# Optimization experiments

Measured on AMD Instinct MI355X. Metric: run time of the kernel, lower is better.

## Reference

```python
import jax, jax.numpy as jnp
import numpy as np
from jax import lax

# --- configuration matching init_kwargs ---
N = 512          # head_size: square cost matrices, marginals a=b=ones(N)
REG = 0.05       # entropy_reg
TAU = 1000.0     # absorption threshold on scaling vectors
N_ITER = 50      # max_iter (fixed iteration count; tol early-exit omitted)
BATCH = 128


def setup_inputs() -> dict:
    key = jax.random.key(0)
    # nonnegative cost matrices, uniform [0,1)
    X = jax.random.uniform(key, (BATCH, N, N), dtype=jnp.float32)
    return {"X": X}


def _sinkhorn_stabilized(M):
    """Log-stabilized Sinkhorn (POT sinkhorn_stabilized) for one cost matrix M [N,N].

    Marginals a = b = ones(N). Returns transport plan Gamma [N,N].
    """
    a = jnp.ones((N,), M.dtype)
    b = jnp.ones((N,), M.dtype)

    def step(carry, _):
        alpha, beta, u, v = carry
        # K = exp(-(M - alpha_i - beta_j)/reg)
        K = jnp.exp((alpha[:, None] + beta[None, :] - M) / REG)
        v = b / (K.T @ u)
        u = a / (K @ v)
        # tau-based absorption of large scalings into the log-domain potentials
        absorb = (jnp.max(jnp.abs(u)) > TAU) | (jnp.max(jnp.abs(v)) > TAU)
        alpha = jnp.where(absorb, alpha + REG * jnp.log(u), alpha)
        beta = jnp.where(absorb, beta + REG * jnp.log(v), beta)
        u = jnp.where(absorb, jnp.full_like(u, 1.0 / N), u)
        v = jnp.where(absorb, jnp.full_like(v, 1.0 / N), v)
        return (alpha, beta, u, v), None

    init = (
        jnp.zeros((N,), M.dtype),          # alpha
        jnp.zeros((N,), M.dtype),          # beta
        jnp.full((N,), 1.0 / N, M.dtype),  # u
        jnp.full((N,), 1.0 / N, M.dtype),  # v
    )
    (alpha, beta, u, v), _ = lax.scan(step, init, None, length=N_ITER)
    # Gamma = exp(-(M - alpha_i - beta_j)/reg + log u_i + log v_j)
    Gamma = jnp.exp(
        (alpha[:, None] + beta[None, :] - M) / REG
        + jnp.log(u)[:, None]
        + jnp.log(v)[None, :]
    )
    return Gamma


def reference(X):
    # original mutates X[i] in place per batch element; we return the batched result
    return jax.vmap(_sinkhorn_stabilized)(X)
```

## Files before the change

kernel.cpp:

```cpp
#include <hip/hip_runtime.h>

constexpr int BN = 512;
constexpr int NITER = 50;

#define CEXP  (-28.853900817779268f)
#define ESH   (14.0f)
#define L2TAU (9.965784284662087f)

typedef unsigned int u32;

__device__ __forceinline__ float fexp2(float x) { return __builtin_amdgcn_exp2f(x); }
__device__ __forceinline__ float flog2(float x) { return __builtin_amdgcn_logf(x); }

__device__ __forceinline__ float nr_rcp(float x) {
    float r = __builtin_amdgcn_rcpf(x);
    return fmaf(r, fmaf(-x, r, 1.0f), r);
}

template <int CTRL>
__device__ __forceinline__ float dppx(float x) {
    return __int_as_float(__builtin_amdgcn_update_dpp(
        0, __float_as_int(x), CTRL, 0xF, 0xF, true));
}

__device__ __forceinline__ float bfly_sum(float x) {
    x += dppx<0xB1>(x);
    x += dppx<0x4E>(x);
    x += dppx<0x141>(x);
    x += dppx<0x140>(x);
    x += __shfl_xor(x, 16, 64);
    x += __shfl_xor(x, 32, 64);
    return x;
}
__device__ __forceinline__ float bfly_max(float x) {
    x = fmaxf(x, dppx<0xB1>(x));
    x = fmaxf(x, dppx<0x4E>(x));
    x = fmaxf(x, dppx<0x141>(x));
    x = fmaxf(x, dppx<0x140>(x));
    x = fmaxf(x, __shfl_xor(x, 16, 64));
    x = fmaxf(x, __shfl_xor(x, 32, 64));
    return x;
}

__device__ __forceinline__ void fma_mix2(float& accLo, float& accHi, u32 e2,
                                         float pLo, float pHi) {
    asm("v_fma_mix_f32 %0, %2, %3, %0 op_sel_hi:[1,0,0]\n\t"
        "v_fma_mix_f32 %1, %2, %4, %1 op_sel:[1,0,0] op_sel_hi:[1,0,0]"
        : "+v"(accLo), "+v"(accHi)
        : "v"(e2), "v"(pLo), "v"(pHi));
}

__global__ __launch_bounds__(256)
void prep_exp_t(const float* __restrict__ X, float* __restrict__ out)
{
    const int blk  = blockIdx.x;
    const int b    = blk >> 4;
    const int tile = blk & 15;
    const int i0   = (tile >> 2) << 7;
    const int j0   = (tile & 3) << 7;
    const int tid  = threadIdx.x;

    const float* __restrict__ Mb = X + (size_t)b * (BN * BN);
    _Float16* __restrict__ Et = reinterpret_cast<_Float16*>(out + (size_t)b * (BN * BN));

    __shared__ _Float16 T[128][130];

    #pragma unroll
    for (int k = 0; k < 16; ++k) {
        int idx = tid + (k << 8);
        int fi  = idx >> 5;
        int fj  = idx & 31;
        float4 m = *reinterpret_cast<const float4*>(Mb + (size_t)(i0 + fi) * BN + j0 + (fj << 2));
        T[(fj << 2) + 0][fi] = (_Float16)fexp2(fmaf(m.x, CEXP, ESH));
        T[(fj << 2) + 1][fi] = (_Float16)fexp2(fmaf(m.y, CEXP, ESH));
        T[(fj << 2) + 2][fi] = (_Float16)fexp2(fmaf(m.z, CEXP, ESH));
        T[(fj << 2) + 3][fi] = (_Float16)fexp2(fmaf(m.w, CEXP, ESH));
    }
    __syncthreads();
    #pragma unroll
    for (int k = 0; k < 32; ++k) {
        int o  = tid + (k << 8);
        int j  = o >> 6;
        int c2 = o & 63;
        u32 val = *reinterpret_cast<const u32*>(&T[j][c2 << 1]);
        *reinterpret_cast<u32*>(Et + (size_t)(j0 + j) * BN + i0 + (c2 << 1)) = val;
    }
}

__global__ __launch_bounds__(1024, 4)
void sinkhorn_iter3(const float* __restrict__ X, float* __restrict__ out,
                    float* __restrict__ cucv)
{
    const int b    = blockIdx.x;
    const int t    = threadIdx.x;
    const int lane = t & 63;
    const int w    = t >> 6;

    const u32* __restrict__ Et4 =
        reinterpret_cast<const u32*>(out + (size_t)b * (BN * BN));

    __shared__ float ah[BN], bh[BN], lu[BN], lv[BN], pv[BN];
    __shared__ float tpart[8][BN];
    __shared__ float wmaxlu[8], wmaxlv[16];
    __shared__ uint4 stage[16][8][64];

    if (t < BN) {
        ah[t] = 0.f; bh[t] = 0.f;
        lu[t] = -9.f; lv[t] = -9.f;
        pv[t] = 0x1p-9f;
    }

    const int jb0 = w << 5;

    #pragma unroll
    for (int c = 0; c < 8; ++c)
        stage[w][c][lane] =
            *reinterpret_cast<const uint4*>(Et4 + (size_t)(jb0 + 24 + c) * 256 + (lane << 2));

    uint4 e[4], f[4];
    #pragma unroll
    for (int c = 0; c < 4; ++c)
        e[c] = *reinterpret_cast<const uint4*>(Et4 + (size_t)(jb0 + c) * 256 + (lane << 2));

    __syncthreads();

    for (int it = 0; it < NITER; ++it) {
        float pr[8];
        *reinterpret_cast<float4*>(&pr[0]) = *reinterpret_cast<const float4*>(&pv[lane * 8]);
        *reinterpret_cast<float4*>(&pr[4]) = *reinterpret_cast<const float4*>(&pv[lane * 8 + 4]);

        float acc[8] = {0, 0, 0, 0, 0, 0, 0, 0};
        float vml = -1e30f;

        auto dogroup = [&](const uint4* eg, int jb) {
            const float4 bh4 = *reinterpret_cast<const float4*>(&bh[jb]);
            float q[4], lvv[4];
            #pragma unroll
            for (int c = 0; c < 4; ++c) {
                float s0 = 0.f, s1 = 0.f;
                fma_mix2(s0, s1, eg[c].x, pr[0], pr[1]);
                fma_mix2(s0, s1, eg[c].y, pr[2], pr[3]);
                fma_mix2(s0, s1, eg[c].z, pr[4], pr[5]);
                fma_mix2(s0, s1, eg[c].w, pr[6], pr[7]);
                float s = bfly_sum(s0 + s1) * 0x1p-14f;
                q[c] = nr_rcp(s);
                const float bj = (c == 0) ? bh4.x : (c == 1) ? bh4.y : (c == 2) ? bh4.z : bh4.w;
                lvv[c] = -bj - flog2(s);
                vml = fmaxf(vml, lvv[c]);
            }
            if (lane == 0)
                *reinterpret_cast<float4*>(&lv[jb]) = make_float4(lvv[0], lvv[1], lvv[2], lvv[3]);
            #pragma unroll
            for (int c = 0; c < 4; ++c) {
                fma_mix2(acc[0], acc[1], eg[c].x, q[c], q[c]);
                fma_mix2(acc[2], acc[3], eg[c].y, q[c], q[c]);
                fma_mix2(acc[4], acc[5], eg[c].z, q[c], q[c]);
                fma_mix2(acc[6], acc[7], eg[c].w, q[c], q[c]);
            }
        };

        #pragma unroll
        for (int g = 0; g < 6; ++g) {
            const int jb = jb0 + (g << 2);
            const int jn = (g < 5) ? (jb + 4) : jb0;
            #pragma unroll
            for (int c = 0; c < 4; ++c)
                f[c] = *reinterpret_cast<const uint4*>(Et4 + (size_t)(jn + c) * 256 + (lane << 2));
            dogroup(e, jb);
            #pragma unroll
            for (int c = 0; c < 4; ++c) e[c] = f[c];
        }
        #pragma unroll
        for (int g = 0; g < 2; ++g) {
            uint4 el[4];
            #pragma unroll
            for (int c = 0; c < 4; ++c) el[c] = stage[w][(g << 2) + c][lane];
            dogroup(el, jb0 + 24 + (g << 2));
        }

        if (w < 8) {
            *reinterpret_cast<float4*>(&tpart[w][lane * 8]) =
                make_float4(acc[0], acc[1], acc[2], acc[3]);
            *reinterpret_cast<float4*>(&tpart[w][lane * 8 + 4]) =
                make_float4(acc[4], acc[5], acc[6], acc[7]);
        }
        if (lane == 0) wmaxlv[w] = vml;
        __syncthreads();
        if (w >= 8) {
            float4* p0 = reinterpret_cast<float4*>(&tpart[w - 8][lane * 8]);
            float4* p1 = reinterpret_cast<float4*>(&tpart[w - 8][lane * 8 + 4]);
            float4 o0 = *p0, o1 = *p1;
            o0.x += acc[0]; o0.y += acc[1]; o0.z += acc[2]; o0.w += acc[3];
            o1.x += acc[4]; o1.y += acc[5]; o1.z += acc[6]; o1.w += acc[7];
            *p0 = o0; *p1 = o1;
        }
        __syncthreads();

        float lun = 0.f, tt = 0.f;
        if (t < BN) {
            float p0 = 0, p1 = 0, p2 = 0, p3 = 0;
            #pragma unroll
            for (int w2 = 0; w2 < 8; w2 += 4) {
                p0 += tpart[w2 + 0][t];
                p1 += tpart[w2 + 1][t];
                p2 += tpart[w2 + 2][t];
                p3 += tpart[w2 + 3][t];
            }
            tt  = ((p0 + p1) + (p2 + p3)) * 0x1p-14f;
            lun = -ah[t] - flog2(tt);
            float m = bfly_max(lun);
            if (lane == 0) wmaxlu[w] = m;
        }
        __syncthreads();

        if (t < BN) {
            float mlu = wmaxlu[0], mlv = wmaxlv[0];
            #pragma unroll
            for (int i2 = 1; i2 < 8; ++i2)  mlu = fmaxf(mlu, wmaxlu[i2]);
            #pragma unroll
            for (int i2 = 1; i2 < 16; ++i2) mlv = fmaxf(mlv, wmaxlv[i2]);
            if (mlu > L2TAU || mlv > L2TAU) {
                float an = ah[t] + lun;
                ah[t] = an;
                lu[t] = -9.f;
                pv[t] = fexp2(an - 9.0f);
                bh[t] += lv[t];
                lv[t] = -9.f;
            } else {
                lu[t] = lun;
                pv[t] = nr_rcp(tt);
            }
        }
        __syncthreads();
    }

    if (cucv != nullptr) {
        if (t < BN) {
            cucv[(size_t)b * 1024 + t]       = ah[t] + lu[t];
            cucv[(size_t)b * 1024 + 512 + t] = bh[t] + lv[t];
        }
    } else {
        if (t < BN) {
            pv[t] = ah[t] + lu[t];
            lv[t] = bh[t] + lv[t];
        }
        __syncthreads();
        const int j  = t & 511;
        const int i0 = (t >> 9) * 256;
        const float cvj = lv[j];
        const float* __restrict__ Mb = X + (size_t)b * (BN * BN);
        float* __restrict__ Gb = out + (size_t)b * (BN * BN);
        #pragma unroll 4
        for (int i = i0; i < i0 + 256; ++i)
            Gb[(size_t)i * BN + j] = fexp2(fmaf(Mb[(size_t)i * BN + j], CEXP, pv[i] + cvj));
    }
}

__global__ __launch_bounds__(256)
void gamma_out(const float* __restrict__ X, float* __restrict__ out,
               const float* __restrict__ cucv)
{
    const int blk  = blockIdx.x;
    const int b    = blk >> 4;
    const int tile = blk & 15;
    const int tid  = threadIdx.x;
    const int i0   = tile << 5;

    __shared__ float cu[32];
    __shared__ float cv[BN];

    if (tid < 32) cu[tid] = cucv[(size_t)b * 1024 + i0 + tid];
    cv[tid]        = cucv[(size_t)b * 1024 + 512 + tid];
    cv[tid + 256]  = cucv[(size_t)b * 1024 + 768 + tid];
    __syncthreads();

    const float* __restrict__ Mb = X + (size_t)b * (BN * BN);
    float* __restrict__ Gb = out + (size_t)b * (BN * BN);
    const float4* __restrict__ cv4 = reinterpret_cast<const float4*>(cv);

    #pragma unroll
    for (int k = 0; k < 16; ++k) {
        int idx = tid + (k << 8);
        int r   = idx >> 7;
        int c4  = idx & 127;
        int i   = i0 + r;
        float4 m = *reinterpret_cast<const float4*>(Mb + (size_t)i * BN + (c4 << 2));
        float4 c = cv4[c4];
        float cui = cu[r];
        float4 g;
        g.x = fexp2(fmaf(m.x, CEXP, cui + c.x));
        g.y = fexp2(fmaf(m.y, CEXP, cui + c.y));
        g.z = fexp2(fmaf(m.z, CEXP, cui + c.z));
        g.w = fexp2(fmaf(m.w, CEXP, cui + c.w));
        *reinterpret_cast<float4*>(Gb + (size_t)i * BN + (c4 << 2)) = g;
    }
}

extern "C" void kernel_launch(void* const* d_in, const int* in_sizes, int n_in,
                              void* d_out, int out_size, void* d_ws, size_t ws_size,
                              hipStream_t stream)
{
    const float* X = (const float*)d_in[0];
    float* out = (float*)d_out;
    const int batch = in_sizes[0] / (BN * BN);

    prep_exp_t<<<batch * 16, 256, 0, stream>>>(X, out);

    const size_t cucv_bytes = (size_t)batch * 1024 * sizeof(float);
    if (ws_size >= cucv_bytes) {
        float* cucv = (float*)d_ws;
        sinkhorn_iter3<<<batch, 1024, 0, stream>>>(X, out, cucv);
        gamma_out<<<batch * 16, 256, 0, stream>>>(X, out, cucv);
    } else {
        sinkhorn_iter3<<<batch, 1024, 0, stream>>>(X, out, nullptr);
    }
}
```

Baseline: 709.2 us.

## Stream E tiles via async global-to-LDS double-buffered loads each iteration

Replaces the register-prefetch-plus-static-LDS-stage scheme with direct global_load_lds double buffering. Every iteration now streams all 8 groups of 4 rows per wave from global or L2 into LDS, instead of keeping a quarter of them resident in LDS. Plain barriers become an explicit lgkmcnt wait plus s_barrier. The aim is to cut VGPR pressure and overlap memory with compute. In exchange it adds more global traffic per iteration, and the vmcnt(4) wait is hand-tuned and could break if the compiler emits other vector-memory ops.

```diff
diff --git a/kernel.cpp b/kernel.cpp
--- a/kernel.cpp
+++ b/kernel.cpp
@@ -48,6 +48,16 @@
         "v_fma_mix_f32 %1, %2, %4, %1 op_sel:[1,0,0] op_sel_hi:[1,0,0]"
         : "+v"(accLo), "+v"(accHi)
         : "v"(e2), "v"(pLo), "v"(pHi));
+}
+
+__device__ __forceinline__ void gload16(const u32* g, void* l) {
+    __builtin_amdgcn_global_load_lds(
+        (const __attribute__((address_space(1))) u32*)g,
+        (__attribute__((address_space(3))) u32*)l, 16, 0, 0);
+}
+
+__device__ __forceinline__ void barrier_lgkm() {
+    asm volatile("s_waitcnt lgkmcnt(0)\n\ts_barrier" ::: "memory");
 }
 
 __global__ __launch_bounds__(256)
@@ -88,7 +98,7 @@
 }
 
 __global__ __launch_bounds__(1024, 4)
-void sinkhorn_iter3(const float* __restrict__ X, float* __restrict__ out,
+void sinkhorn_iter4(const float* __restrict__ X, float* __restrict__ out,
                     float* __restrict__ cucv)
 {
     const int b    = blockIdx.x;
@@ -102,27 +112,21 @@
     __shared__ float ah[BN], bh[BN], lu[BN], lv[BN], pv[BN];
     __shared__ float tpart[8][BN];
     __shared__ float wmaxlu[8], wmaxlv[16];
-    __shared__ uint4 stage[16][8][64];
+    __shared__ uint4 sbuf[16][2][4][64];
 
     if (t < BN) {
         ah[t] = 0.f; bh[t] = 0.f;
         lu[t] = -9.f; lv[t] = -9.f;
         pv[t] = 0x1p-9f;
     }
+    __syncthreads();
 
     const int jb0 = w << 5;
-
-    #pragma unroll
-    for (int c = 0; c < 8; ++c)
-        stage[w][c][lane] =
-            *reinterpret_cast<const uint4*>(Et4 + (size_t)(jb0 + 24 + c) * 256 + (lane << 2));
-
-    uint4 e[4], f[4];
+    const u32* gb = Et4 + (size_t)jb0 * 256 + (lane << 2);
+
     #pragma unroll
     for (int c = 0; c < 4; ++c)
-        e[c] = *reinterpret_cast<const uint4*>(Et4 + (size_t)(jb0 + c) * 256 + (lane << 2));
-
-    __syncthreads();
+        gload16(gb + c * 256, &sbuf[w][0][c][0]);
 
     for (int it = 0; it < NITER; ++it) {
         float pr[8];
@@ -132,50 +136,44 @@
         float acc[8] = {0, 0, 0, 0, 0, 0, 0, 0};
         float vml = -1e30f;
 
-        auto dogroup = [&](const uint4* eg, int jb) {
+        #pragma unroll
+        for (int g = 0; g < 8; ++g) {
+            const int nb   = (g + 1) & 7;
+            const int nbuf = (g + 1) & 1;
+            #pragma unroll
+            for (int c = 0; c < 4; ++c)
+                gload16(gb + (size_t)(nb * 4 + c) * 256, &sbuf[w][nbuf][c][0]);
+
+            asm volatile("s_waitcnt vmcnt(4)" ::: "memory");
+
+            const int jb = jb0 + (g << 2);
+            uint4 e[4];
+            #pragma unroll
+            for (int c = 0; c < 4; ++c) e[c] = sbuf[w][g & 1][c][lane];
+
             const float4 bh4 = *reinterpret_cast<const float4*>(&bh[jb]);
-            float q[4], lvv[4];
+            float q[4];
             #pragma unroll
             for (int c = 0; c < 4; ++c) {
                 float s0 = 0.f, s1 = 0.f;
-                fma_mix2(s0, s1, eg[c].x, pr[0], pr[1]);
-                fma_mix2(s0, s1, eg[c].y, pr[2], pr[3]);
-                fma_mix2(s0, s1, eg[c].z, pr[4], pr[5]);
-                fma_mix2(s0, s1, eg[c].w, pr[6], pr[7]);
+                fma_mix2(s0, s1, e[c].x, pr[0], pr[1]);
+                fma_mix2(s0, s1, e[c].y, pr[2], pr[3]);
+                fma_mix2(s0, s1, e[c].z, pr[4], pr[5]);
+                fma_mix2(s0, s1, e[c].w, pr[6], pr[7]);
                 float s = bfly_sum(s0 + s1) * 0x1p-14f;
                 q[c] = nr_rcp(s);
                 const float bj = (c == 0) ? bh4.x : (c == 1) ? bh4.y : (c == 2) ? bh4.z : bh4.w;
-                lvv[c] = -bj - flog2(s);
-                vml = fmaxf(vml, lvv[c]);
+                float lvj = -bj - flog2(s);
+                vml = fmaxf(vml, lvj);
+                if (lane == 0) lv[jb + c] = lvj;
             }
-            if (lane == 0)
-                *reinterpret_cast<float4*>(&lv[jb]) = make_float4(lvv[0], lvv[1], lvv[2], lvv[3]);
             #pragma unroll
             for (int c = 0; c < 4; ++c) {
-                fma_mix2(acc[0], acc[1], eg[c].x, q[c], q[c]);
-                fma_mix2(acc[2], acc[3], eg[c].y, q[c], q[c]);
-                fma_mix2(acc[4], acc[5], eg[c].z, q[c], q[c]);
-                fma_mix2(acc[6], acc[7], eg[c].w, q[c], q[c]);
+                fma_mix2(acc[0], acc[1], e[c].x, q[c], q[c]);
+                fma_mix2(acc[2], acc[3], e[c].y, q[c], q[c]);
+                fma_mix2(acc[4], acc[5], e[c].z, q[c], q[c]);
+                fma_mix2(acc[6], acc[7], e[c].w, q[c], q[c]);
             }
-        };
-
-        #pragma unroll
-        for (int g = 0; g < 6; ++g) {
-            const int jb = jb0 + (g << 2);
-            const int jn = (g < 5) ? (jb + 4) : jb0;
-            #pragma unroll
-            for (int c = 0; c < 4; ++c)
-                f[c] = *reinterpret_cast<const uint4*>(Et4 + (size_t)(jn + c) * 256 + (lane << 2));
-            dogroup(e, jb);
-            #pragma unroll
-            for (int c = 0; c < 4; ++c) e[c] = f[c];
-        }
-        #pragma unroll
-        for (int g = 0; g < 2; ++g) {
-            uint4 el[4];
-            #pragma unroll
-            for (int c = 0; c < 4; ++c) el[c] = stage[w][(g << 2) + c][lane];
-            dogroup(el, jb0 + 24 + (g << 2));
         }
 
         if (w < 8) {
@@ -185,7 +183,7 @@
                 make_float4(acc[4], acc[5], acc[6], acc[7]);
         }
         if (lane == 0) wmaxlv[w] = vml;
-        __syncthreads();
+        barrier_lgkm();
         if (w >= 8) {
             float4* p0 = reinterpret_cast<float4*>(&tpart[w - 8][lane * 8]);
             float4* p1 = reinterpret_cast<float4*>(&tpart[w - 8][lane * 8 + 4]);
@@ -194,7 +192,7 @@
             o1.x += acc[4]; o1.y += acc[5]; o1.z += acc[6]; o1.w += acc[7];
             *p0 = o0; *p1 = o1;
         }
-        __syncthreads();
+        barrier_lgkm();
 
         float lun = 0.f, tt = 0.f;
         if (t < BN) {
@@ -211,7 +209,7 @@
             float m = bfly_max(lun);
             if (lane == 0) wmaxlu[w] = m;
         }
-        __syncthreads();
+        barrier_lgkm();
 
         if (t < BN) {
             float mlu = wmaxlu[0], mlv = wmaxlv[0];
@@ -231,8 +229,10 @@
                 pv[t] = nr_rcp(tt);
             }
         }
-        __syncthreads();
-    }
+        barrier_lgkm();
+    }
+
+    asm volatile("s_waitcnt vmcnt(0)" ::: "memory");
 
     if (cucv != nullptr) {
         if (t < BN) {
@@ -309,9 +309,9 @@
     const size_t cucv_bytes = (size_t)batch * 1024 * sizeof(float);
     if (ws_size >= cucv_bytes) {
         float* cucv = (float*)d_ws;
-        sinkhorn_iter3<<<batch, 1024, 0, stream>>>(X, out, cucv);
+        sinkhorn_iter4<<<batch, 1024, 0, stream>>>(X, out, cucv);
         gamma_out<<<batch * 16, 256, 0, stream>>>(X, out, cucv);
     } else {
-        sinkhorn_iter3<<<batch, 1024, 0, stream>>>(X, out, nullptr);
-    }
-}
+        sinkhorn_iter4<<<batch, 1024, 0, stream>>>(X, out, nullptr);
+    }
+}
```

Result: slower. 900.9 us (+27.0%).

## Deepen global prefetch ring, shrink LDS staging, drop a barrier per iteration

Applied to the files above, without the earlier changes.

The per-wave matrix loop now keeps a three-group-deep register ring of prefetched global loads instead of a single double buffer. Fewer rows are staged in LDS (4 instead of 8), so more are streamed from global or L2 each iteration. All 16 waves write their partial column sums into a larger LDS buffer, which removes one barrier and the read-add-write reduction step. Barriers become a raw lgkmcnt wait plus s_barrier, and occupancy is pinned with waves_per_eu(4,4). The trade-off is higher register pressure from the ring and more global traffic per iteration, in exchange for more latency hiding and less synchronization.

```diff
diff --git a/kernel.cpp b/kernel.cpp
--- a/kernel.cpp
+++ b/kernel.cpp
@@ -48,6 +48,10 @@
         "v_fma_mix_f32 %1, %2, %4, %1 op_sel:[1,0,0] op_sel_hi:[1,0,0]"
         : "+v"(accLo), "+v"(accHi)
         : "v"(e2), "v"(pLo), "v"(pHi));
+}
+
+__device__ __forceinline__ void barrier_lgkm() {
+    asm volatile("s_waitcnt lgkmcnt(0)\n\ts_barrier" ::: "memory");
 }
 
 __global__ __launch_bounds__(256)
@@ -87,8 +91,9 @@
     }
 }
 
-__global__ __launch_bounds__(1024, 4)
-void sinkhorn_iter3(const float* __restrict__ X, float* __restrict__ out,
+__global__ __launch_bounds__(1024)
+__attribute__((amdgpu_waves_per_eu(4, 4)))
+void sinkhorn_iter5(const float* __restrict__ X, float* __restrict__ out,
                     float* __restrict__ cucv)
 {
     const int b    = blockIdx.x;
@@ -100,9 +105,9 @@
         reinterpret_cast<const u32*>(out + (size_t)b * (BN * BN));
 
     __shared__ float ah[BN], bh[BN], lu[BN], lv[BN], pv[BN];
-    __shared__ float tpart[8][BN];
+    __shared__ float tpart[16][BN];
     __shared__ float wmaxlu[8], wmaxlv[16];
-    __shared__ uint4 stage[16][8][64];
+    __shared__ uint4 stage[16][4][64];
 
     if (t < BN) {
         ah[t] = 0.f; bh[t] = 0.f;
@@ -113,14 +118,17 @@
     const int jb0 = w << 5;
 
     #pragma unroll
-    for (int c = 0; c < 8; ++c)
+    for (int c = 0; c < 4; ++c)
         stage[w][c][lane] =
-            *reinterpret_cast<const uint4*>(Et4 + (size_t)(jb0 + 24 + c) * 256 + (lane << 2));
-
-    uint4 e[4], f[4];
-    #pragma unroll
-    for (int c = 0; c < 4; ++c)
-        e[c] = *reinterpret_cast<const uint4*>(Et4 + (size_t)(jb0 + c) * 256 + (lane << 2));
+            *reinterpret_cast<const uint4*>(Et4 + (size_t)(jb0 + 28 + c) * 256 + (lane << 2));
+
+    uint4 ring[4][4];
+    #pragma unroll
+    for (int g = 0; g < 3; ++g)
+        #pragma unroll
+        for (int c = 0; c < 4; ++c)
+            ring[g][c] = *reinterpret_cast<const uint4*>(
+                Et4 + (size_t)(jb0 + (g << 2) + c) * 256 + (lane << 2));
 
     __syncthreads();
 
@@ -134,7 +142,7 @@
 
         auto dogroup = [&](const uint4* eg, int jb) {
             const float4 bh4 = *reinterpret_cast<const float4*>(&bh[jb]);
-            float q[4], lvv[4];
+            float q[4];
             #pragma unroll
             for (int c = 0; c < 4; ++c) {
                 float s0 = 0.f, s1 = 0.f;
@@ -145,11 +153,10 @@
                 float s = bfly_sum(s0 + s1) * 0x1p-14f;
                 q[c] = nr_rcp(s);
                 const float bj = (c == 0) ? bh4.x : (c == 1) ? bh4.y : (c == 2) ? bh4.z : bh4.w;
-                lvv[c] = -bj - flog2(s);
-                vml = fmaxf(vml, lvv[c]);
+                float lvj = -bj - flog2(s);
+                vml = fmaxf(vml, lvj);
+                if (lane == 0) lv[jb + c] = lvj;
             }
-            if (lane == 0)
-                *reinterpret_cast<float4*>(&lv[jb]) = make_float4(lvv[0], lvv[1], lvv[2], lvv[3]);
             #pragma unroll
             for (int c = 0; c < 4; ++c) {
                 fma_mix2(acc[0], acc[1], eg[c].x, q[c], q[c]);
@@ -160,47 +167,33 @@
         };
 
         #pragma unroll
-        for (int g = 0; g < 6; ++g) {
-            const int jb = jb0 + (g << 2);
-            const int jn = (g < 5) ? (jb + 4) : jb0;
+        for (int g = 0; g < 7; ++g) {
+            dogroup(ring[g & 3], jb0 + (g << 2));
+            const int gp = (g + 3) % 7;
             #pragma unroll
             for (int c = 0; c < 4; ++c)
-                f[c] = *reinterpret_cast<const uint4*>(Et4 + (size_t)(jn + c) * 256 + (lane << 2));
-            dogroup(e, jb);
-            #pragma unroll
-            for (int c = 0; c < 4; ++c) e[c] = f[c];
-        }
-        #pragma unroll
-        for (int g = 0; g < 2; ++g) {
+                ring[gp & 3][c] = *reinterpret_cast<const uint4*>(
+                    Et4 + (size_t)(jb0 + (gp << 2) + c) * 256 + (lane << 2));
+        }
+        {
             uint4 el[4];
             #pragma unroll
-            for (int c = 0; c < 4; ++c) el[c] = stage[w][(g << 2) + c][lane];
-            dogroup(el, jb0 + 24 + (g << 2));
-        }
-
-        if (w < 8) {
-            *reinterpret_cast<float4*>(&tpart[w][lane * 8]) =
-                make_float4(acc[0], acc[1], acc[2], acc[3]);
-            *reinterpret_cast<float4*>(&tpart[w][lane * 8 + 4]) =
-                make_float4(acc[4], acc[5], acc[6], acc[7]);
-        }
+            for (int c = 0; c < 4; ++c) el[c] = stage[w][c][lane];
+            dogroup(el, jb0 + 28);
+        }
+
+        *reinterpret_cast<float4*>(&tpart[w][lane * 8]) =
+            make_float4(acc[0], acc[1], acc[2], acc[3]);
+        *reinterpret_cast<float4*>(&tpart[w][lane * 8 + 4]) =
+            make_float4(acc[4], acc[5], acc[6], acc[7]);
         if (lane == 0) wmaxlv[w] = vml;
-        __syncthreads();
-        if (w >= 8) {
-            float4* p0 = reinterpret_cast<float4*>(&tpart[w - 8][lane * 8]);
-            float4* p1 = reinterpret_cast<float4*>(&tpart[w - 8][lane * 8 + 4]);
-            float4 o0 = *p0, o1 = *p1;
-            o0.x += acc[0]; o0.y += acc[1]; o0.z += acc[2]; o0.w += acc[3];
-            o1.x += acc[4]; o1.y += acc[5]; o1.z += acc[6]; o1.w += acc[7];
-            *p0 = o0; *p1 = o1;
-        }
-        __syncthreads();
+        barrier_lgkm();
 
         float lun = 0.f, tt = 0.f;
         if (t < BN) {
             float p0 = 0, p1 = 0, p2 = 0, p3 = 0;
             #pragma unroll
-            for (int w2 = 0; w2 < 8; w2 += 4) {
+            for (int w2 = 0; w2 < 16; w2 += 4) {
                 p0 += tpart[w2 + 0][t];
                 p1 += tpart[w2 + 1][t];
                 p2 += tpart[w2 + 2][t];
@@ -211,7 +204,7 @@
             float m = bfly_max(lun);
             if (lane == 0) wmaxlu[w] = m;
         }
-        __syncthreads();
+        barrier_lgkm();
 
         if (t < BN) {
             float mlu = wmaxlu[0], mlv = wmaxlv[0];
@@ -231,7 +224,7 @@
                 pv[t] = nr_rcp(tt);
             }
         }
-        __syncthreads();
+        barrier_lgkm();
     }
 
     if (cucv != nullptr) {
@@ -309,9 +302,9 @@
     const size_t cucv_bytes = (size_t)batch * 1024 * sizeof(float);
     if (ws_size >= cucv_bytes) {
         float* cucv = (float*)d_ws;
-        sinkhorn_iter3<<<batch, 1024, 0, stream>>>(X, out, cucv);
+        sinkhorn_iter5<<<batch, 1024, 0, stream>>>(X, out, cucv);
         gamma_out<<<batch * 16, 256, 0, stream>>>(X, out, cucv);
     } else {
-        sinkhorn_iter3<<<batch, 1024, 0, stream>>>(X, out, nullptr);
-    }
-}
+        sinkhorn_iter5<<<batch, 1024, 0, stream>>>(X, out, nullptr);
+    }
+}
```

New measurement: 918.1 us. 1.29x slower.

## Add register-resident sinkhorn kernel with deep global prefetch, dropping LDS staging

Applied to the files above, without the earlier changes.

Adds a new sinkhorn_deep kernel that keeps the whole per-wave slice of the exp matrix streaming through four rotating register groups. Each group is prefetched from global memory three steps ahead, replacing the shared-memory staging buffer. It lowers launch bounds to 2 blocks per CU to allow more registers, and uses 16-way partial sums plus raw lgkmcnt barriers. A host check on the compiled register count selects between the new kernel and the old one. The cost is that every iteration re-reads the matrix from L2/global instead of part of it staying in LDS, and occupancy is lower.

```diff
diff --git a/kernel.cpp b/kernel.cpp
--- a/kernel.cpp
+++ b/kernel.cpp
@@ -48,6 +48,10 @@
         "v_fma_mix_f32 %1, %2, %4, %1 op_sel:[1,0,0] op_sel_hi:[1,0,0]"
         : "+v"(accLo), "+v"(accHi)
         : "v"(e2), "v"(pLo), "v"(pHi));
+}
+
+__device__ __forceinline__ void barrier_lgkm() {
+    asm volatile("s_waitcnt lgkmcnt(0)\n\ts_barrier" ::: "memory");
 }
 
 __global__ __launch_bounds__(256)
@@ -87,9 +91,56 @@
     }
 }
 
-__global__ __launch_bounds__(1024, 4)
-void sinkhorn_iter3(const float* __restrict__ X, float* __restrict__ out,
-                    float* __restrict__ cucv)
+__device__ __forceinline__ void consume4(
+    uint4 c0, uint4 c1, uint4 c2, uint4 c3, int jb,
+    float pr0, float pr1, float pr2, float pr3,
+    float pr4, float pr5, float pr6, float pr7,
+    float& a0, float& a1, float& a2, float& a3,
+    float& a4, float& a5, float& a6, float& a7,
+    float& vml, const float* bh, float* lv, int lane)
+{
+    const float4 bh4 = *reinterpret_cast<const float4*>(&bh[jb]);
+
+    float s00 = 0.f, s01 = 0.f;
+    fma_mix2(s00, s01, c0.x, pr0, pr1); fma_mix2(s00, s01, c0.y, pr2, pr3);
+    fma_mix2(s00, s01, c0.z, pr4, pr5); fma_mix2(s00, s01, c0.w, pr6, pr7);
+    float s10 = 0.f, s11 = 0.f;
+    fma_mix2(s10, s11, c1.x, pr0, pr1); fma_mix2(s10, s11, c1.y, pr2, pr3);
+    fma_mix2(s10, s11, c1.z, pr4, pr5); fma_mix2(s10, s11, c1.w, pr6, pr7);
+    float s20 = 0.f, s21 = 0.f;
+    fma_mix2(s20, s21, c2.x, pr0, pr1); fma_mix2(s20, s21, c2.y, pr2, pr3);
+    fma_mix2(s20, s21, c2.z, pr4, pr5); fma_mix2(s20, s21, c2.w, pr6, pr7);
+    float s30 = 0.f, s31 = 0.f;
+    fma_mix2(s30, s31, c3.x, pr0, pr1); fma_mix2(s30, s31, c3.y, pr2, pr3);
+    fma_mix2(s30, s31, c3.z, pr4, pr5); fma_mix2(s30, s31, c3.w, pr6, pr7);
+
+    float r0 = bfly_sum(s00 + s01);
+    float r1 = bfly_sum(s10 + s11);
+    float r2 = bfly_sum(s20 + s21);
+    float r3 = bfly_sum(s30 + s31);
+
+    float t0 = r0 * 0x1p-14f, t1 = r1 * 0x1p-14f;
+    float t2 = r2 * 0x1p-14f, t3 = r3 * 0x1p-14f;
+    float q0 = nr_rcp(t0), q1 = nr_rcp(t1), q2 = nr_rcp(t2), q3 = nr_rcp(t3);
+    float l0 = -bh4.x - flog2(t0), l1 = -bh4.y - flog2(t1);
+    float l2 = -bh4.z - flog2(t2), l3 = -bh4.w - flog2(t3);
+    vml = fmaxf(vml, fmaxf(fmaxf(l0, l1), fmaxf(l2, l3)));
+    if (lane == 0)
+        *reinterpret_cast<float4*>(&lv[jb]) = make_float4(l0, l1, l2, l3);
+
+    fma_mix2(a0, a1, c0.x, q0, q0); fma_mix2(a2, a3, c0.y, q0, q0);
+    fma_mix2(a4, a5, c0.z, q0, q0); fma_mix2(a6, a7, c0.w, q0, q0);
+    fma_mix2(a0, a1, c1.x, q1, q1); fma_mix2(a2, a3, c1.y, q1, q1);
+    fma_mix2(a4, a5, c1.z, q1, q1); fma_mix2(a6, a7, c1.w, q1, q1);
+    fma_mix2(a0, a1, c2.x, q2, q2); fma_mix2(a2, a3, c2.y, q2, q2);
+    fma_mix2(a4, a5, c2.z, q2, q2); fma_mix2(a6, a7, c2.w, q2, q2);
+    fma_mix2(a0, a1, c3.x, q3, q3); fma_mix2(a2, a3, c3.y, q3, q3);
+    fma_mix2(a4, a5, c3.z, q3, q3); fma_mix2(a6, a7, c3.w, q3, q3);
+}
+
+__global__ __launch_bounds__(1024, 2)
+void sinkhorn_deep(const float* __restrict__ X, float* __restrict__ out,
+                   float* __restrict__ cucv)
 {
     const int b    = blockIdx.x;
     const int t    = threadIdx.x;
@@ -100,9 +151,8 @@
         reinterpret_cast<const u32*>(out + (size_t)b * (BN * BN));
 
     __shared__ float ah[BN], bh[BN], lu[BN], lv[BN], pv[BN];
-    __shared__ float tpart[8][BN];
+    __shared__ float tpart[16][BN];
     __shared__ float wmaxlu[8], wmaxlv[16];
-    __shared__ uint4 stage[16][8][64];
 
     if (t < BN) {
         ah[t] = 0.f; bh[t] = 0.f;
@@ -111,6 +161,117 @@
     }
 
     const int jb0 = w << 5;
+    const u32* gbase = Et4 + (size_t)jb0 * 256 + (lane << 2);
+#define LD(c) (*reinterpret_cast<const uint4*>(gbase + (size_t)(c) * 256))
+
+    uint4 e0 = LD(0),  e1 = LD(1),  e2 = LD(2),  e3 = LD(3);
+    uint4 f0 = LD(4),  f1 = LD(5),  f2 = LD(6),  f3 = LD(7);
+    uint4 h0 = LD(8),  h1 = LD(9),  h2 = LD(10), h3 = LD(11);
+    uint4 k0, k1, k2, k3;
+
+    __syncthreads();
+
+    for (int it = 0; it < NITER; ++it) {
+        const float4 prA = *reinterpret_cast<const float4*>(&pv[lane * 8]);
+        const float4 prB = *reinterpret_cast<const float4*>(&pv[lane * 8 + 4]);
+        const float pr0 = prA.x, pr1 = prA.y, pr2 = prA.z, pr3 = prA.w;
+        const float pr4 = prB.x, pr5 = prB.y, pr6 = prB.z, pr7 = prB.w;
+
+        float a0 = 0.f, a1 = 0.f, a2 = 0.f, a3 = 0.f;
+        float a4 = 0.f, a5 = 0.f, a6 = 0.f, a7 = 0.f;
+        float vml = -1e30f;
+
+#define STEP(B0,B1,B2,B3, I0,I1,I2,I3, ICOL, JOFF)                            \
+        I0 = LD((ICOL) + 0); I1 = LD((ICOL) + 1);                             \
+        I2 = LD((ICOL) + 2); I3 = LD((ICOL) + 3);                             \
+        consume4(B0, B1, B2, B3, jb0 + (JOFF),                                \
+                 pr0, pr1, pr2, pr3, pr4, pr5, pr6, pr7,                      \
+                 a0, a1, a2, a3, a4, a5, a6, a7, vml, bh, lv, lane);
+
+        STEP(e0,e1,e2,e3, k0,k1,k2,k3, 12,  0)
+        STEP(f0,f1,f2,f3, e0,e1,e2,e3, 16,  4)
+        STEP(h0,h1,h2,h3, f0,f1,f2,f3, 20,  8)
+        STEP(k0,k1,k2,k3, h0,h1,h2,h3, 24, 12)
+        STEP(e0,e1,e2,e3, k0,k1,k2,k3, 28, 16)
+        STEP(f0,f1,f2,f3, e0,e1,e2,e3,  0, 20)
+        STEP(h0,h1,h2,h3, f0,f1,f2,f3,  4, 24)
+        STEP(k0,k1,k2,k3, h0,h1,h2,h3,  8, 28)
+#undef STEP
+
+        *reinterpret_cast<float4*>(&tpart[w][lane * 8]) = make_float4(a0, a1, a2, a3);
+        *reinterpret_cast<float4*>(&tpart[w][lane * 8 + 4]) = make_float4(a4, a5, a6, a7);
+        if (lane == 0) wmaxlv[w] = vml;
+        barrier_lgkm();
+
+        float lun = 0.f, tt = 0.f;
+        if (t < BN) {
+            float p0 = 0, p1 = 0, p2 = 0, p3 = 0;
+            #pragma unroll
+            for (int w2 = 0; w2 < 16; w2 += 4) {
+                p0 += tpart[w2 + 0][t];
+                p1 += tpart[w2 + 1][t];
+                p2 += tpart[w2 + 2][t];
+                p3 += tpart[w2 + 3][t];
+            }
+            tt  = ((p0 + p1) + (p2 + p3)) * 0x1p-14f;
+            lun = -ah[t] - flog2(tt);
+            float m = bfly_max(lun);
+            if (lane == 0) wmaxlu[w] = m;
+        }
+        barrier_lgkm();
+
+        if (t < BN) {
+            float mlu = wmaxlu[0], mlv = wmaxlv[0];
+            #pragma unroll
+            for (int i2 = 1; i2 < 8; ++i2)  mlu = fmaxf(mlu, wmaxlu[i2]);
+            #pragma unroll
+            for (int i2 = 1; i2 < 16; ++i2) mlv = fmaxf(mlv, wmaxlv[i2]);
+            if (mlu > L2TAU || mlv > L2TAU) {
+                float an = ah[t] + lun;
+                ah[t] = an;
+                lu[t] = -9.f;
+                pv[t] = fexp2(an - 9.0f);
+                bh[t] += lv[t];
+                lv[t] = -9.f;
+            } else {
+                lu[t] = lun;
+                pv[t] = nr_rcp(tt);
+            }
+        }
+        barrier_lgkm();
+    }
+#undef LD
+
+    if (t < BN) {
+        cucv[(size_t)b * 1024 + t]       = ah[t] + lu[t];
+        cucv[(size_t)b * 1024 + 512 + t] = bh[t] + lv[t];
+    }
+}
+
+__global__ __launch_bounds__(1024, 4)
+void sinkhorn_iter3(const float* __restrict__ X, float* __restrict__ out,
+                    float* __restrict__ cucv)
+{
+    const int b    = blockIdx.x;
+    const int t    = threadIdx.x;
+    const int lane = t & 63;
+    const int w    = t >> 6;
+
+    const u32* __restrict__ Et4 =
+        reinterpret_cast<const u32*>(out + (size_t)b * (BN * BN));
+
+    __shared__ float ah[BN], bh[BN], lu[BN], lv[BN], pv[BN];
+    __shared__ float tpart[8][BN];
+    __shared__ float wmaxlu[8], wmaxlv[16];
+    __shared__ uint4 stage[16][8][64];
+
+    if (t < BN) {
+        ah[t] = 0.f; bh[t] = 0.f;
+        lu[t] = -9.f; lv[t] = -9.f;
+        pv[t] = 0x1p-9f;
+    }
+
+    const int jb0 = w << 5;
 
     #pragma unroll
     for (int c = 0; c < 8; ++c)
@@ -134,7 +295,7 @@
 
         auto dogroup = [&](const uint4* eg, int jb) {
             const float4 bh4 = *reinterpret_cast<const float4*>(&bh[jb]);
-            float q[4], lvv[4];
+            float q[4];
             #pragma unroll
             for (int c = 0; c < 4; ++c) {
                 float s0 = 0.f, s1 = 0.f;
@@ -145,11 +306,10 @@
                 float s = bfly_sum(s0 + s1) * 0x1p-14f;
                 q[c] = nr_rcp(s);
                 const float bj = (c == 0) ? bh4.x : (c == 1) ? bh4.y : (c == 2) ? bh4.z : bh4.w;
-                lvv[c] = -bj - flog2(s);
-                vml = fmaxf(vml, lvv[c]);
-            }
-            if (lane == 0)
-                *reinterpret_cast<float4*>(&lv[jb]) = make_float4(lvv[0], lvv[1], lvv[2], lvv[3]);
+                float lvj = -bj - flog2(s);
+                vml = fmaxf(vml, lvj);
+                if (lane == 0) lv[jb + c] = lvj;
+            }
             #pragma unroll
             for (int c = 0; c < 4; ++c) {
                 fma_mix2(acc[0], acc[1], eg[c].x, q[c], q[c]);
@@ -306,10 +466,18 @@
 
     prep_exp_t<<<batch * 16, 256, 0, stream>>>(X, out);
 
+    bool deep_ok = false;
+    hipFuncAttributes fa{};
+    if (hipFuncGetAttributes(&fa, (const void*)sinkhorn_deep) == hipSuccess)
+        deep_ok = (fa.numRegs >= 80 && fa.numRegs <= 160);
+
     const size_t cucv_bytes = (size_t)batch * 1024 * sizeof(float);
     if (ws_size >= cucv_bytes) {
         float* cucv = (float*)d_ws;
-        sinkhorn_iter3<<<batch, 1024, 0, stream>>>(X, out, cucv);
+        if (deep_ok)
+            sinkhorn_deep<<<batch, 1024, 0, stream>>>(X, out, cucv);
+        else
+            sinkhorn_iter3<<<batch, 1024, 0, stream>>>(X, out, cucv);
         gamma_out<<<batch * 16, 256, 0, stream>>>(X, out, cucv);
     } else {
         sinkhorn_iter3<<<batch, 1024, 0, stream>>>(X, out, nullptr);
```

New measurement: 1.125 ms. 58.6% more time.
